# Kernel tuning notes

Hardware: AMD Instinct MI355X
Metric: run time of the kernel (lower is better)

## Reference

```python
import jax, jax.numpy as jnp
import numpy as np

EPS = 1e-5
SLOPE = 0.2


def _edge_conv(x, w, gamma, beta, k):
    # x: (B,N,D); w: (O, 2D); returns (B,N,O)
    sq = jnp.sum(x * x, axis=-1)                                  # (B,N)
    # negative squared distance: larger = closer
    neg = 2.0 * jnp.einsum('bnd,bmd->bnm', x, x) - sq[:, :, None] - sq[:, None, :]
    _, idx = jax.lax.top_k(neg, k + 1)                            # (B,N,k+1)
    idx = idx[:, :, 1:]                                           # drop self -> (B,N,k)
    neigh = jax.vmap(lambda xb, ib: xb[ib])(x, idx)               # (B,N,k,D)
    ctr = jnp.broadcast_to(x[:, :, None, :], neigh.shape)
    edge = jnp.concatenate([neigh - ctr, ctr], axis=-1)           # (B,N,k,2D)
    h = jnp.einsum('bnkc,oc->bnko', edge, w)                      # 1x1 conv
    h = h * (gamma / jnp.sqrt(1.0 + EPS)) + beta                  # BN eval (mean=0,var=1)
    h = jnp.where(h > 0, h, SLOPE * h)                            # LeakyReLU(0.2)
    return jnp.max(h, axis=2)                                     # max over k -> (B,N,O)


def _bn_eval(x, gamma, beta):
    return x * (gamma / jnp.sqrt(1.0 + EPS)) + beta


def _lrelu(x):
    return jnp.where(x > 0, x, SLOPE * x)


def setup_inputs() -> dict:
    key = jax.random.key(0)
    ks = jax.random.split(key, 32)
    B, N, D, k, num_classes = 4, 4096, 3, 10, 3
    s = 0.1
    inp = {
        'points': jax.random.normal(ks[0], (B, N, D), jnp.float32),
        'k': k,
        'w1': jax.random.normal(ks[1], (64, 6), jnp.float32) * s,
        'g1': 1.0 + 0.1 * jax.random.normal(ks[2], (64,), jnp.float32),
        'b1': 0.1 * jax.random.normal(ks[3], (64,), jnp.float32),
        'w2': jax.random.normal(ks[4], (64, 128), jnp.float32) * s,
        'g2': 1.0 + 0.1 * jax.random.normal(ks[5], (64,), jnp.float32),
        'b2': 0.1 * jax.random.normal(ks[6], (64,), jnp.float32),
        'w3': jax.random.normal(ks[7], (128, 128), jnp.float32) * s,
        'g3': 1.0 + 0.1 * jax.random.normal(ks[8], (128,), jnp.float32),
        'b3': 0.1 * jax.random.normal(ks[9], (128,), jnp.float32),
        'w4': jax.random.normal(ks[10], (256, 256), jnp.float32) * s,
        'g4': 1.0 + 0.1 * jax.random.normal(ks[11], (256,), jnp.float32),
        'b4': 0.1 * jax.random.normal(ks[12], (256,), jnp.float32),
        'w5': jax.random.normal(ks[13], (1024, 512), jnp.float32) * s,
        'g5': 1.0 + 0.1 * jax.random.normal(ks[14], (1024,), jnp.float32),
        'b5': 0.1 * jax.random.normal(ks[15], (1024,), jnp.float32),
        'fw1': jax.random.normal(ks[16], (512, 1024), jnp.float32) * s,
        'fg1': 1.0 + 0.1 * jax.random.normal(ks[17], (512,), jnp.float32),
        'fbt1': 0.1 * jax.random.normal(ks[18], (512,), jnp.float32),
        'fw2': jax.random.normal(ks[19], (256, 512), jnp.float32) * s,
        'fb2': 0.1 * jax.random.normal(ks[20], (256,), jnp.float32),
        'fg2': 1.0 + 0.1 * jax.random.normal(ks[21], (256,), jnp.float32),
        'fbt2': 0.1 * jax.random.normal(ks[22], (256,), jnp.float32),
        'fw3': jax.random.normal(ks[23], (num_classes, 256), jnp.float32) * s,
        'fb3': 0.1 * jax.random.normal(ks[24], (num_classes,), jnp.float32),
    }
    return inp


def reference(points, w1, g1, b1, w2, g2, b2, w3, g3, b3, w4, g4, b4,
              w5, g5, b5, fw1, fg1, fbt1, fw2, fb2, fg2, fbt2, fw3, fb3, k):
    o1 = _edge_conv(points, w1, g1, b1, k)   # (B,N,64)
    o2 = _edge_conv(o1, w2, g2, b2, k)       # (B,N,64)
    o3 = _edge_conv(o2, w3, g3, b3, k)       # (B,N,128)
    o4 = _edge_conv(o3, w4, g4, b4, k)       # (B,N,256)
    cat = jnp.concatenate([o1, o2, o3, o4], axis=-1)   # (B,N,512)
    h = jnp.einsum('bnc,oc->bno', cat, w5)   # (B,N,1024)
    h = _lrelu(_bn_eval(h, g5, b5))
    h = jnp.max(h, axis=1)                   # global max over N -> (B,1024)
    # fc head (dropout = identity in eval)
    h = _lrelu(_bn_eval(h @ fw1.T, fg1, fbt1))
    h = _lrelu(_bn_eval(h @ fw2.T + fb2, fg2, fbt2))
    out = h @ fw3.T + fb3                    # (B,num_classes)
    return out
```

## Files before the change

kernel.cpp:

```cpp
#include <hip/hip_runtime.h>
#include <math.h>

#define N_PTS 4096
#define BATCH 4
#define KNN 10

__device__ __forceinline__ bool better(float v1, int i1, float v2, int i2) {
    return (v1 > v2) || (v1 == v2 && i1 < i2);
}

__device__ __forceinline__ unsigned f2key(float x) {
    unsigned u = __float_as_uint(x);
    return (u & 0x80000000u) ? ~u : (u | 0x80000000u);
}
__device__ __forceinline__ float key2f(unsigned k) {
    unsigned u = (k & 0x80000000u) ? (k & 0x7FFFFFFFu) : ~k;
    return __uint_as_float(u);
}

__device__ __forceinline__ float lrelu(float h) { return (h > 0.f) ? h : 0.2f * h; }

__device__ __forceinline__ unsigned long long pack_kd(float v, int c) {
    return ((unsigned long long)f2key(v) << 32) | (unsigned)~(unsigned)c;
}

__device__ __forceinline__ unsigned long long bcast64(unsigned long long x, int src) {
    unsigned lo = (unsigned)__builtin_amdgcn_readlane((int)(unsigned)(x & 0xFFFFFFFFu), src);
    unsigned hi = (unsigned)__builtin_amdgcn_readlane((int)(unsigned)(x >> 32), src);
    return ((unsigned long long)hi << 32) | lo;
}

__global__ void sq_kernel(const float* __restrict__ x, int xstr, int D,
                          float* __restrict__ sq) {
    int g = blockIdx.x * blockDim.x + threadIdx.x;
    if (g >= BATCH * N_PTS) return;
    const float* row = x + (long)g * xstr;
    float s = 0.f;
    if ((D & 3) == 0) {
        for (int c = 0; c < D; c += 4) {
            float4 v = *(const float4*)&row[c];
            s += v.x * v.x + v.y * v.y + v.z * v.z + v.w * v.w;
        }
    } else {
        for (int c = 0; c < D; ++c) { float v = row[c]; s += v * v; }
    }
    sq[g] = s;
}

__global__ __launch_bounds__(256) void dist_kernel(const float* __restrict__ x,
                                                   const float* __restrict__ sq,
                                                   float* __restrict__ dist,
                                                   int xstr, int D, int row0) {
    __shared__ float As[16][132];
    __shared__ float Bs[16][132];
    int b = blockIdx.z;
    const float* xb = x + (long)b * N_PTS * xstr;
    const float* sqb = sq + b * N_PTS;
    float* db = dist + (long)b * 1024 * N_PTS;
    int r0 = row0 + blockIdx.y * 128;
    int c0 = blockIdx.x * 128;
    int tx = threadIdx.x & 15, ty = threadIdx.x >> 4;
    float acc[8][8] = {};
    int nk = (D + 15) >> 4;
    for (int kt = 0; kt < nk; ++kt) {
        int k0 = kt * 16;
        for (int e = threadIdx.x; e < 2048; e += 256) {
            int kk = e & 15, r = e >> 4;
            int c = k0 + kk;
            As[kk][r] = (c < D) ? xb[(long)(r0 + r) * xstr + c] : 0.f;
            Bs[kk][r] = (c < D) ? xb[(long)(c0 + r) * xstr + c] : 0.f;
        }
        __syncthreads();
        #pragma unroll
        for (int kk = 0; kk < 16; ++kk) {
            float a[8], bb[8];
            *(float4*)&a[0] = *(float4*)&As[kk][ty * 8];
            *(float4*)&a[4] = *(float4*)&As[kk][ty * 8 + 4];
            *(float4*)&bb[0] = *(float4*)&Bs[kk][tx * 8];
            *(float4*)&bb[4] = *(float4*)&Bs[kk][tx * 8 + 4];
            #pragma unroll
            for (int i = 0; i < 8; ++i)
                #pragma unroll
                for (int j = 0; j < 8; ++j) acc[i][j] += a[i] * bb[j];
        }
        __syncthreads();
    }
    #pragma unroll
    for (int i = 0; i < 8; ++i) {
        int lr = blockIdx.y * 128 + ty * 8 + i;
        float sr = sqb[r0 + ty * 8 + i];
        int cb = c0 + tx * 8;
        float4 v0, v1;
        v0.x = 2.f * acc[i][0] - sr - sqb[cb + 0];
        v0.y = 2.f * acc[i][1] - sr - sqb[cb + 1];
        v0.z = 2.f * acc[i][2] - sr - sqb[cb + 2];
        v0.w = 2.f * acc[i][3] - sr - sqb[cb + 3];
        v1.x = 2.f * acc[i][4] - sr - sqb[cb + 4];
        v1.y = 2.f * acc[i][5] - sr - sqb[cb + 5];
        v1.z = 2.f * acc[i][6] - sr - sqb[cb + 6];
        v1.w = 2.f * acc[i][7] - sr - sqb[cb + 7];
        *(float4*)&db[(long)lr * N_PTS + cb] = v0;
        *(float4*)&db[(long)lr * N_PTS + cb + 4] = v1;
    }
}

__global__ __launch_bounds__(256) void topk_kernel(const float* __restrict__ dist,
                                                   int* __restrict__ idxout, int row0) {
    int b = blockIdx.y;
    int wave = threadIdx.x >> 6;
    int lane = threadIdx.x & 63;
    int row_local = blockIdx.x * 4 + wave;
    const float4* d4 =
        (const float4*)(dist + (long)b * 1024 * N_PTS + (long)row_local * N_PTS);

    unsigned long long elem = 0ull;
    unsigned long long T = 0ull;
    float Tf = -INFINITY;

    float4 cur = d4[lane];
    for (int jj = 0; jj < 16; ++jj) {
        float4 nxt;
        if (jj < 15) nxt = d4[(jj + 1) * 64 + lane];
        float vmax = fmaxf(fmaxf(cur.x, cur.y), fmaxf(cur.z, cur.w));
        if (__ballot(vmax >= Tf)) {
            int cbase = jj * 256 + lane * 4;
            unsigned long long kc[4];
            kc[0] = pack_kd(cur.x, cbase + 0);
            kc[1] = pack_kd(cur.y, cbase + 1);
            kc[2] = pack_kd(cur.z, cbase + 2);
            kc[3] = pack_kd(cur.w, cbase + 3);
            #pragma unroll
            for (int q = 0; q < 4; ++q) {
                unsigned long long kq = kc[q];
                unsigned long long mask;
                while ((mask = __ballot(kq > T)) != 0ull) {
                    int src = __ffsll(mask) - 1;
                    unsigned long long kb = bcast64(kq, src);
                    if (lane == src) kq = 0ull;
                    unsigned long long below = __ballot(elem > kb);
                    int pos = __popcll(below);
                    unsigned long long prev = __shfl_up(elem, 1);
                    if (lane == pos) elem = kb;
                    else if (lane > pos && lane <= 10) elem = prev;
                    T = bcast64(elem, 10);
                    Tf = key2f((unsigned)(T >> 32));
                }
            }
        }
        cur = nxt;
    }
    if (lane >= 1 && lane <= 10) {
        int c = (int)~(unsigned)(elem & 0xFFFFFFFFu);
        idxout[((long)b * N_PTS + row0 + row_local) * KNN + (lane - 1)] = c;
    }
}

template <int DIN, int DOUT, int PTS, int TPP>
__global__ __launch_bounds__(256) void edgeconv_kernel(
    const float* __restrict__ x, int xstr, const int* __restrict__ idx,
    const float* __restrict__ w, const float* __restrict__ gamma,
    const float* __restrict__ beta, float* __restrict__ out, int outoff) {
    constexpr int DP = DIN + 1;
    constexpr int C2 = 2 * DIN;
    __shared__ float ctr[PTS][DP];
    __shared__ float nm[PTS][KNN][DP];
    int p0 = blockIdx.x * PTS;
    for (int e = threadIdx.x; e < PTS * DIN; e += 256) {
        int p = e / DIN, c = e - p * DIN;
        ctr[p][c] = x[(long)(p0 + p) * xstr + c];
    }
    __syncthreads();
    for (int e = threadIdx.x; e < PTS * KNN * DIN; e += 256) {
        int p = e / (KNN * DIN);
        int rem = e - p * (KNN * DIN);
        int kk = rem / DIN, c = rem - kk * DIN;
        int g = p0 + p;
        int nb = (g & ~(N_PTS - 1)) + idx[(long)g * KNN + kk];
        nm[p][kk][c] = x[(long)nb * xstr + c] - ctr[p][c];
    }
    __syncthreads();
    int p = threadIdx.x / TPP;
    int og = (threadIdx.x % TPP) * 4;
    float gs[4], bt[4];
    #pragma unroll
    for (int j = 0; j < 4; ++j) {
        gs[j] = gamma[og + j] / sqrtf(1.f + 1e-5f);
        bt[j] = beta[og + j];
    }
    float base[4] = {0.f, 0.f, 0.f, 0.f};
    for (int c = 0; c < DIN; ++c) {
        float cv = ctr[p][c];
        #pragma unroll
        for (int j = 0; j < 4; ++j) base[j] += cv * w[(og + j) * C2 + DIN + c];
    }
    float acc[KNN][4];
    #pragma unroll
    for (int kk = 0; kk < KNN; ++kk)
        #pragma unroll
        for (int j = 0; j < 4; ++j) acc[kk][j] = base[j];
    for (int c = 0; c < DIN; ++c) {
        float w4[4];
        #pragma unroll
        for (int j = 0; j < 4; ++j) w4[j] = w[(og + j) * C2 + c];
        #pragma unroll
        for (int kk = 0; kk < KNN; ++kk) {
            float nv = nm[p][kk][c];
            #pragma unroll
            for (int j = 0; j < 4; ++j) acc[kk][j] += nv * w4[j];
        }
    }
    float best[4] = {-INFINITY, -INFINITY, -INFINITY, -INFINITY};
    #pragma unroll
    for (int kk = 0; kk < KNN; ++kk)
        #pragma unroll
        for (int j = 0; j < 4; ++j)
            best[j] = fmaxf(best[j], lrelu(acc[kk][j] * gs[j] + bt[j]));
    #pragma unroll
    for (int j = 0; j < 4; ++j)
        out[(long)(p0 + p) * 512 + outoff + og + j] = best[j];
}

template <int DIN, int DOUT>
__global__ __launch_bounds__(256) void uvgemm_kernel(
    const float* __restrict__ x, int xoff, const float* __restrict__ w,
    float* __restrict__ uv) {
    constexpr int NC = 2 * DOUT;
    __shared__ float As[16][132];
    __shared__ float Bs[16][132];
    int r0 = blockIdx.y * 128;
    int c0 = blockIdx.x * 128;
    int tx = threadIdx.x & 15, ty = threadIdx.x >> 4;
    float acc[8][8] = {};
    #pragma unroll 1
    for (int kt = 0; kt < DIN / 16; ++kt) {
        int k0 = kt * 16;
        for (int e = threadIdx.x; e < 2048; e += 256) {
            int kk = e & 15, r = e >> 4;
            As[kk][r] = x[(long)(r0 + r) * 512 + xoff + k0 + kk];
            int jg = c0 + r;
            Bs[kk][r] = (jg < DOUT) ? w[(long)jg * (2 * DIN) + k0 + kk]
                                    : w[(long)(jg - DOUT) * (2 * DIN) + DIN + k0 + kk];
        }
        __syncthreads();
        #pragma unroll
        for (int kk = 0; kk < 16; ++kk) {
            float a[8], bb[8];
            *(float4*)&a[0] = *(float4*)&As[kk][ty * 8];
            *(float4*)&a[4] = *(float4*)&As[kk][ty * 8 + 4];
            *(float4*)&bb[0] = *(float4*)&Bs[kk][tx * 8];
            *(float4*)&bb[4] = *(float4*)&Bs[kk][tx * 8 + 4];
            #pragma unroll
            for (int i = 0; i < 8; ++i)
                #pragma unroll
                for (int j = 0; j < 8; ++j) acc[i][j] += a[i] * bb[j];
        }
        __syncthreads();
    }
    #pragma unroll
    for (int i = 0; i < 8; ++i) {
        int r = r0 + ty * 8 + i;
        int cb = c0 + tx * 8;
        *(float4*)&uv[(long)r * NC + cb] = *(float4*)&acc[i][0];
        *(float4*)&uv[(long)r * NC + cb + 4] = *(float4*)&acc[i][4];
    }
}

template <int DOUT>
__global__ __launch_bounds__(256) void edgemax_kernel(
    const float* __restrict__ uv, const int* __restrict__ idx,
    const float* __restrict__ gamma, const float* __restrict__ beta,
    float* __restrict__ out, int outoff) {
    constexpr int NC = 2 * DOUT;
    constexpr int TPP = DOUT / 4;
    constexpr int TP = 256 / TPP;
    __shared__ int sidx[TP][KNN];
    int p0 = blockIdx.x * TP;
    for (int e = threadIdx.x; e < TP * KNN; e += 256)
        sidx[e / KNN][e % KNN] = idx[(long)(p0 + e / KNN) * KNN + (e % KNN)];
    __syncthreads();
    int p = threadIdx.x / TPP;
    int og = (threadIdx.x % TPP) * 4;
    int g = p0 + p;
    int base_pt = g & ~(N_PTS - 1);
    const float* rowg = uv + (long)g * NC;
    float4 u_n = *(const float4*)&rowg[og];
    float4 v_n = *(const float4*)&rowg[DOUT + og];
    float c0 = v_n.x - u_n.x, c1 = v_n.y - u_n.y;
    float c2 = v_n.z - u_n.z, c3 = v_n.w - u_n.w;
    const float rs = 1.f / sqrtf(1.f + 1e-5f);
    float gs0 = gamma[og + 0] * rs, gs1 = gamma[og + 1] * rs;
    float gs2 = gamma[og + 2] * rs, gs3 = gamma[og + 3] * rs;
    float bt0 = beta[og + 0], bt1 = beta[og + 1];
    float bt2 = beta[og + 2], bt3 = beta[og + 3];
    float b0 = -INFINITY, b1 = -INFINITY, b2 = -INFINITY, b3 = -INFINITY;
    #pragma unroll
    for (int kk = 0; kk < KNN; ++kk) {
        int nb = base_pt + sidx[p][kk];
        float4 ub = *(const float4*)&uv[(long)nb * NC + og];
        b0 = fmaxf(b0, lrelu((ub.x + c0) * gs0 + bt0));
        b1 = fmaxf(b1, lrelu((ub.y + c1) * gs1 + bt1));
        b2 = fmaxf(b2, lrelu((ub.z + c2) * gs2 + bt2));
        b3 = fmaxf(b3, lrelu((ub.w + c3) * gs3 + bt3));
    }
    float4 o4; o4.x = b0; o4.y = b1; o4.z = b2; o4.w = b3;
    *(float4*)&out[(long)g * 512 + outoff + og] = o4;
}

__global__ void init_h5_kernel(unsigned* __restrict__ h5key) {
    int t = blockIdx.x * blockDim.x + threadIdx.x;
    if (t < BATCH * 1024) h5key[t] = 0u;
}

__global__ __launch_bounds__(256) void w5max_kernel(
    const float* __restrict__ cat, const float* __restrict__ w5,
    const float* __restrict__ g5, const float* __restrict__ b5,
    unsigned* __restrict__ h5key) {
    __shared__ float As[16][132];
    __shared__ float Bs[16][132];
    int b = blockIdx.z;
    int n0 = blockIdx.y * 128, o0 = blockIdx.x * 128;
    int tx = threadIdx.x & 15, ty = threadIdx.x >> 4;
    const float* A = cat + (long)b * N_PTS * 512;
    float acc[8][8] = {};
    for (int kt = 0; kt < 32; ++kt) {
        int k0 = kt * 16;
        for (int e = threadIdx.x; e < 2048; e += 256) {
            int kk = e & 15, r = e >> 4;
            As[kk][r] = A[(long)(n0 + r) * 512 + k0 + kk];
            Bs[kk][r] = w5[(long)(o0 + r) * 512 + k0 + kk];
        }
        __syncthreads();
        #pragma unroll
        for (int kk = 0; kk < 16; ++kk) {
            float a[8], bb[8];
            *(float4*)&a[0] = *(float4*)&As[kk][ty * 8];
            *(float4*)&a[4] = *(float4*)&As[kk][ty * 8 + 4];
            *(float4*)&bb[0] = *(float4*)&Bs[kk][tx * 8];
            *(float4*)&bb[4] = *(float4*)&Bs[kk][tx * 8 + 4];
            #pragma unroll
            for (int i = 0; i < 8; ++i)
                #pragma unroll
                for (int j = 0; j < 8; ++j) acc[i][j] += a[i] * bb[j];
        }
        __syncthreads();
    }
    float colmax[8];
    #pragma unroll
    for (int j = 0; j < 8; ++j) {
        int o = o0 + tx * 8 + j;
        float gsc = g5[o] / sqrtf(1.f + 1e-5f);
        float bto = b5[o];
        float m = -INFINITY;
        #pragma unroll
        for (int i = 0; i < 8; ++i)
            m = fmaxf(m, lrelu(acc[i][j] * gsc + bto));
        colmax[j] = m;
    }
    __syncthreads();
    float* red = &As[0][0];
    #pragma unroll
    for (int j = 0; j < 8; ++j) red[ty * 128 + tx * 8 + j] = colmax[j];
    __syncthreads();
    if (threadIdx.x < 128) {
        int col = threadIdx.x;
        float m = -INFINITY;
        #pragma unroll
        for (int t = 0; t < 16; ++t) m = fmaxf(m, red[t * 128 + col]);
        atomicMax(&h5key[b * 1024 + o0 + col], f2key(m));
    }
}

__global__ void fc1_kernel(const unsigned* __restrict__ h5key,
                           const float* __restrict__ fw1,
                           const float* __restrict__ fg1,
                           const float* __restrict__ fbt1,
                           float* __restrict__ f1) {
    int o = blockIdx.x * 256 + threadIdx.x;
    int b = blockIdx.y;
    if (o >= 512) return;
    float s = 0.f;
    for (int c = 0; c < 1024; ++c)
        s += key2f(h5key[b * 1024 + c]) * fw1[o * 1024 + c];
    float h = s * (fg1[o] / sqrtf(1.f + 1e-5f)) + fbt1[o];
    f1[b * 512 + o] = lrelu(h);
}

__global__ void fc2_kernel(const float* __restrict__ f1,
                           const float* __restrict__ fw2,
                           const float* __restrict__ fb2,
                           const float* __restrict__ fg2,
                           const float* __restrict__ fbt2,
                           float* __restrict__ f2) {
    int o = threadIdx.x;
    int b = blockIdx.x;
    float s = fb2[o];
    for (int c = 0; c < 512; ++c) s += f1[b * 512 + c] * fw2[o * 512 + c];
    float h = s * (fg2[o] / sqrtf(1.f + 1e-5f)) + fbt2[o];
    f2[b * 256 + o] = lrelu(h);
}

__global__ void fc3_kernel(const float* __restrict__ f2,
                           const float* __restrict__ fw3,
                           const float* __restrict__ fb3,
                           float* __restrict__ out) {
    int t = threadIdx.x;
    if (t >= BATCH * 3) return;
    int b = t / 3, o = t - b * 3;
    float s = fb3[o];
    for (int c = 0; c < 256; ++c) s += f2[b * 256 + c] * fw3[o * 256 + c];
    out[t] = s;
}

extern "C" void kernel_launch(void* const* d_in, const int* in_sizes, int n_in,
                              void* d_out, int out_size, void* d_ws, size_t ws_size,
                              hipStream_t stream) {
    const float* points = (const float*)d_in[0];
    const float* w1 = (const float*)d_in[2];
    const float* g1 = (const float*)d_in[3];
    const float* b1 = (const float*)d_in[4];
    const float* w2 = (const float*)d_in[5];
    const float* g2 = (const float*)d_in[6];
    const float* b2 = (const float*)d_in[7];
    const float* w3 = (const float*)d_in[8];
    const float* g3 = (const float*)d_in[9];
    const float* b3 = (const float*)d_in[10];
    const float* w4 = (const float*)d_in[11];
    const float* g4 = (const float*)d_in[12];
    const float* b4 = (const float*)d_in[13];
    const float* w5 = (const float*)d_in[14];
    const float* g5 = (const float*)d_in[15];
    const float* b5 = (const float*)d_in[16];
    const float* fw1 = (const float*)d_in[17];
    const float* fg1 = (const float*)d_in[18];
    const float* fbt1 = (const float*)d_in[19];
    const float* fw2 = (const float*)d_in[20];
    const float* fb2 = (const float*)d_in[21];
    const float* fg2 = (const float*)d_in[22];
    const float* fbt2 = (const float*)d_in[23];
    const float* fw3 = (const float*)d_in[24];
    const float* fb3 = (const float*)d_in[25];

    float* ws = (float*)d_ws;
    float* cat = ws;
    float* sq = cat + (long)BATCH * N_PTS * 512;
    unsigned* h5key = (unsigned*)(sq + BATCH * N_PTS);
    float* f1 = (float*)(h5key + BATCH * 1024);
    float* f2 = f1 + BATCH * 512;
    int* idxbuf = (int*)(f2 + BATCH * 256);
    float* dist = (float*)(idxbuf + (long)BATCH * N_PTS * KNN);
    float* uv = dist;

    auto knn = [&](const float* xbase, int xstr, int D) {
        sq_kernel<<<64, 256, 0, stream>>>(xbase, xstr, D, sq);
        for (int r0 = 0; r0 < N_PTS; r0 += 1024) {
            dist_kernel<<<dim3(32, 8, BATCH), 256, 0, stream>>>(xbase, sq, dist, xstr, D, r0);
            topk_kernel<<<dim3(256, BATCH), 256, 0, stream>>>(dist, idxbuf, r0);
        }
    };

    knn(points, 3, 3);
    edgeconv_kernel<3, 64, 16, 16><<<N_PTS * BATCH / 16, 256, 0, stream>>>(
        points, 3, idxbuf, w1, g1, b1, cat, 0);

    knn(cat + 0, 512, 64);
    uvgemm_kernel<64, 64><<<dim3(1, 128), 256, 0, stream>>>(cat, 0, w2, uv);
    edgemax_kernel<64><<<1024, 256, 0, stream>>>(uv, idxbuf, g2, b2, cat, 64);

    knn(cat + 64, 512, 64);
    uvgemm_kernel<64, 128><<<dim3(2, 128), 256, 0, stream>>>(cat, 64, w3, uv);
    edgemax_kernel<128><<<2048, 256, 0, stream>>>(uv, idxbuf, g3, b3, cat, 128);

    knn(cat + 128, 512, 128);
    uvgemm_kernel<128, 256><<<dim3(4, 128), 256, 0, stream>>>(cat, 128, w4, uv);
    edgemax_kernel<256><<<4096, 256, 0, stream>>>(uv, idxbuf, g4, b4, cat, 256);

    init_h5_kernel<<<16, 256, 0, stream>>>(h5key);
    w5max_kernel<<<dim3(8, 32, BATCH), 256, 0, stream>>>(cat, w5, g5, b5, h5key);

    fc1_kernel<<<dim3(2, BATCH), 256, 0, stream>>>(h5key, fw1, fg1, fbt1, f1);
    fc2_kernel<<<BATCH, 256, 0, stream>>>(f1, fw2, fb2, fg2, fbt2, f2);
    fc3_kernel<<<1, 64, 0, stream>>>(f2, fw3, fb3, (float*)d_out);
}
```

Measured before the change: 1.831 ms.

## Compute full symmetric distance matrix once and run top-k in one pass

When the workspace can hold the full 4096x4096 distance matrix per batch, a new kernel computes only the upper-triangle 128x128 tiles and writes each tile plus its transpose through shared memory. This halves the dot-product work. The four row-chunk dist/topk launch pairs become one distance launch and one top-k launch. The new top-k kernel prefetches four float4 values at a time to deepen memory-level parallelism. The cost is a much larger workspace footprint, plus transposed writes that go through shared memory with extra syncs.

```diff
diff --git a/kernel.cpp b/kernel.cpp
--- a/kernel.cpp
+++ b/kernel.cpp
@@ -4,10 +4,6 @@
 #define N_PTS 4096
 #define BATCH 4
 #define KNN 10
-
-__device__ __forceinline__ bool better(float v1, int i1, float v2, int i2) {
-    return (v1 > v2) || (v1 == v2 && i1 < i2);
-}
 
 __device__ __forceinline__ unsigned f2key(float x) {
     unsigned u = __float_as_uint(x);
@@ -104,6 +100,90 @@
     }
 }
 
+__global__ __launch_bounds__(256) void distsym_kernel(const float* __restrict__ x,
+                                                      const float* __restrict__ sq,
+                                                      float* __restrict__ dist,
+                                                      int xstr, int D) {
+    __shared__ float As[16][132];
+    __shared__ float Bs[16][132];
+    __shared__ float Tt[64][132];
+    int b = blockIdx.z;
+    int t = blockIdx.x, br = 0;
+    while (t >= 32 - br) { t -= 32 - br; ++br; }
+    int bc = br + t;
+    const float* xb = x + (long)b * N_PTS * xstr;
+    const float* sqb = sq + b * N_PTS;
+    float* db = dist + (long)b * N_PTS * N_PTS;
+    int r0 = br * 128, c0 = bc * 128;
+    int tx = threadIdx.x & 15, ty = threadIdx.x >> 4;
+    float acc[8][8] = {};
+    int nk = (D + 15) >> 4;
+    for (int kt = 0; kt < nk; ++kt) {
+        int k0 = kt * 16;
+        for (int e = threadIdx.x; e < 2048; e += 256) {
+            int kk = e & 15, r = e >> 4;
+            int c = k0 + kk;
+            As[kk][r] = (c < D) ? xb[(long)(r0 + r) * xstr + c] : 0.f;
+            Bs[kk][r] = (c < D) ? xb[(long)(c0 + r) * xstr + c] : 0.f;
+        }
+        __syncthreads();
+        #pragma unroll
+        for (int kk = 0; kk < 16; ++kk) {
+            float a[8], bb[8];
+            *(float4*)&a[0] = *(float4*)&As[kk][ty * 8];
+            *(float4*)&a[4] = *(float4*)&As[kk][ty * 8 + 4];
+            *(float4*)&bb[0] = *(float4*)&Bs[kk][tx * 8];
+            *(float4*)&bb[4] = *(float4*)&Bs[kk][tx * 8 + 4];
+            #pragma unroll
+            for (int i = 0; i < 8; ++i)
+                #pragma unroll
+                for (int j = 0; j < 8; ++j) acc[i][j] += a[i] * bb[j];
+        }
+        __syncthreads();
+    }
+    float sqr[8], sqc[8];
+    #pragma unroll
+    for (int i = 0; i < 8; ++i) sqr[i] = sqb[r0 + ty * 8 + i];
+    #pragma unroll
+    for (int j = 0; j < 8; ++j) sqc[j] = sqb[c0 + tx * 8 + j];
+    #pragma unroll
+    for (int i = 0; i < 8; ++i) {
+        int R = r0 + ty * 8 + i;
+        int cb = c0 + tx * 8;
+        float4 v0, v1;
+        v0.x = 2.f * acc[i][0] - sqr[i] - sqc[0];
+        v0.y = 2.f * acc[i][1] - sqr[i] - sqc[1];
+        v0.z = 2.f * acc[i][2] - sqr[i] - sqc[2];
+        v0.w = 2.f * acc[i][3] - sqr[i] - sqc[3];
+        v1.x = 2.f * acc[i][4] - sqr[i] - sqc[4];
+        v1.y = 2.f * acc[i][5] - sqr[i] - sqc[5];
+        v1.z = 2.f * acc[i][6] - sqr[i] - sqc[6];
+        v1.w = 2.f * acc[i][7] - sqr[i] - sqc[7];
+        *(float4*)&db[(long)R * N_PTS + cb] = v0;
+        *(float4*)&db[(long)R * N_PTS + cb + 4] = v1;
+    }
+    if (br == bc) return;
+    #pragma unroll
+    for (int h = 0; h < 2; ++h) {
+        __syncthreads();
+        if ((tx >> 3) == h) {
+            int txl = tx & 7;
+            #pragma unroll
+            for (int j = 0; j < 8; ++j)
+                #pragma unroll
+                for (int i = 0; i < 8; ++i)
+                    Tt[txl * 8 + j][ty * 8 + i] =
+                        (2.f * acc[i][j] - sqc[j]) - sqr[i];
+        }
+        __syncthreads();
+        for (int e = threadIdx.x; e < 2048; e += 256) {
+            int rr = e >> 5, cc = (e & 31) << 2;
+            *(float4*)&db[(long)(c0 + h * 64 + rr) * N_PTS + r0 + cc] =
+                *(const float4*)&Tt[rr][cc];
+        }
+    }
+}
+
 __global__ __launch_bounds__(256) void topk_kernel(const float* __restrict__ dist,
                                                    int* __restrict__ idxout, int row0) {
     int b = blockIdx.y;
@@ -152,6 +232,67 @@
     if (lane >= 1 && lane <= 10) {
         int c = (int)~(unsigned)(elem & 0xFFFFFFFFu);
         idxout[((long)b * N_PTS + row0 + row_local) * KNN + (lane - 1)] = c;
+    }
+}
+
+__global__ __launch_bounds__(256) void topkfull_kernel(const float* __restrict__ dist,
+                                                       int* __restrict__ idxout) {
+    int b = blockIdx.y;
+    int wave = threadIdx.x >> 6;
+    int lane = threadIdx.x & 63;
+    int row = blockIdx.x * 4 + wave;
+    const float4* d4 =
+        (const float4*)(dist + (long)b * N_PTS * N_PTS + (long)row * N_PTS);
+
+    unsigned long long elem = 0ull;
+    unsigned long long T = 0ull;
+    float Tf = -INFINITY;
+
+    float4 buf[4];
+    #pragma unroll
+    for (int p = 0; p < 4; ++p) buf[p] = d4[p * 64 + lane];
+    for (int base = 0; base < 16; base += 4) {
+        float4 nbuf[4];
+        if (base + 4 < 16) {
+            #pragma unroll
+            for (int p = 0; p < 4; ++p) nbuf[p] = d4[(base + 4 + p) * 64 + lane];
+        }
+        #pragma unroll
+        for (int p = 0; p < 4; ++p) {
+            float4 cur = buf[p];
+            float vmax = fmaxf(fmaxf(cur.x, cur.y), fmaxf(cur.z, cur.w));
+            if (__ballot(vmax >= Tf)) {
+                int cbase = (base + p) * 256 + lane * 4;
+                unsigned long long kc[4];
+                kc[0] = pack_kd(cur.x, cbase + 0);
+                kc[1] = pack_kd(cur.y, cbase + 1);
+                kc[2] = pack_kd(cur.z, cbase + 2);
+                kc[3] = pack_kd(cur.w, cbase + 3);
+                #pragma unroll
+                for (int q = 0; q < 4; ++q) {
+                    unsigned long long kq = kc[q];
+                    unsigned long long mask;
+                    while ((mask = __ballot(kq > T)) != 0ull) {
+                        int src = __ffsll(mask) - 1;
+                        unsigned long long kb = bcast64(kq, src);
+                        if (lane == src) kq = 0ull;
+                        unsigned long long below = __ballot(elem > kb);
+                        int pos = __popcll(below);
+                        unsigned long long prev = __shfl_up(elem, 1);
+                        if (lane == pos) elem = kb;
+                        else if (lane > pos && lane <= 10) elem = prev;
+                        T = bcast64(elem, 10);
+                        Tf = key2f((unsigned)(T >> 32));
+                    }
+                }
+            }
+        }
+        #pragma unroll
+        for (int p = 0; p < 4; ++p) buf[p] = nbuf[p];
+    }
+    if (lane >= 1 && lane <= 10) {
+        int c = (int)~(unsigned)(elem & 0xFFFFFFFFu);
+        idxout[((long)b * N_PTS + row) * KNN + (lane - 1)] = c;
     }
 }
 
@@ -450,11 +591,22 @@
     float* dist = (float*)(idxbuf + (long)BATCH * N_PTS * KNN);
     float* uv = dist;
 
+    size_t need = (size_t)((char*)(dist + (size_t)BATCH * N_PTS * N_PTS) -
+                           (char*)d_ws);
+    bool fullp = ws_size >= need;
+
     auto knn = [&](const float* xbase, int xstr, int D) {
         sq_kernel<<<64, 256, 0, stream>>>(xbase, xstr, D, sq);
-        for (int r0 = 0; r0 < N_PTS; r0 += 1024) {
-            dist_kernel<<<dim3(32, 8, BATCH), 256, 0, stream>>>(xbase, sq, dist, xstr, D, r0);
-            topk_kernel<<<dim3(256, BATCH), 256, 0, stream>>>(dist, idxbuf, r0);
+        if (fullp) {
+            distsym_kernel<<<dim3(528, 1, BATCH), 256, 0, stream>>>(
+                xbase, sq, dist, xstr, D);
+            topkfull_kernel<<<dim3(N_PTS / 4, BATCH), 256, 0, stream>>>(dist, idxbuf);
+        } else {
+            for (int r0 = 0; r0 < N_PTS; r0 += 1024) {
+                dist_kernel<<<dim3(32, 8, BATCH), 256, 0, stream>>>(xbase, sq, dist,
+                                                                    xstr, D, r0);
+                topk_kernel<<<dim3(256, BATCH), 256, 0, stream>>>(dist, idxbuf, r0);
+            }
         }
     };
 
```

After: 1.783 ms. 2.6% less time.
